# Kernel tuning notes

Measured on AMD Instinct MI355X. Metric: run time of the kernel, lower is better.

## Reference

```python
import jax, jax.numpy as jnp
import numpy as np


def setup_inputs() -> dict:
    key = jax.random.key(0)
    k1, k2, k3, k4, k5, k6 = jax.random.split(key, 6)
    B, N, D, H = 32, 4096, 256, 256
    return {
        "queries": jax.random.normal(k1, (B, N, D), dtype=jnp.float32),
        "keys": jax.random.normal(k2, (B, N, D), dtype=jnp.float32),
        "values": jax.random.normal(k3, (B, N, D), dtype=jnp.float32),
        "Wq": jax.random.normal(k4, (H, D), dtype=jnp.float32) * (1.0 / np.sqrt(D)),
        "Wk": jax.random.normal(k5, (H, D), dtype=jnp.float32) * (1.0 / np.sqrt(D)),
        "Wv": jax.random.normal(k6, (1, H), dtype=jnp.float32) * (1.0 / np.sqrt(H)),
    }


def reference(queries, keys, values, Wq, Wk, Wv):
    # Project queries and keys to hidden dim (torch Linear weight is [out, in])
    q = jnp.einsum('bnd,hd->bnh', queries, Wq)   # [B, N, H]
    k = jnp.einsum('bnd,hd->bnh', keys, Wk)      # [B, N, H]
    features = jnp.tanh(q + k)                   # [B, N, H]
    scores = jnp.einsum('bnh,oh->bno', features, Wv)  # [B, N, 1]
    alpha = jax.nn.softmax(scores, axis=1)       # softmax over N
    # dropout p=0 -> identity
    aggr_max = jnp.argmax(alpha, axis=1)         # [B, 1]
    out = jnp.sum(alpha * values, axis=1)        # [B, D]
    return (out, aggr_max)
```

## Files before the change

kernel.cpp:

```cpp
#include <hip/hip_runtime.h>

#define Bb 32
#define Nn 4096
#define Dd 256
#define Hh 256
#define NCH 32
#define CHUNK 128
#define NSTEPS 16

typedef __attribute__((ext_vector_type(8))) short bf16x8;
typedef __attribute__((ext_vector_type(4))) float f32x4;

__device__ __forceinline__ unsigned short bf16_rtn(float x) {
    unsigned int u = __float_as_uint(x);
    u += 0x7FFF + ((u >> 16) & 1);
    return (unsigned short)(u >> 16);
}
__device__ __forceinline__ float bf16_to_f(unsigned short b) {
    return __uint_as_float(((unsigned int)b) << 16);
}
__device__ __forceinline__ float fast_tanhf(float x) {
    float e = __expf(2.0f * x);
    return 1.0f - 2.0f / (e + 1.0f);
}

__device__ __forceinline__ void split8_store(short* hp, short* lp, f32x4 v0, f32x4 v1) {
    float xs[8] = {v0.x, v0.y, v0.z, v0.w, v1.x, v1.y, v1.z, v1.w};
    unsigned int hu[4], lu[4];
#pragma unroll
    for (int p = 0; p < 4; ++p) {
        unsigned int u0 = __float_as_uint(xs[2 * p]);
        unsigned int u1 = __float_as_uint(xs[2 * p + 1]);
        float r0 = xs[2 * p]     - __uint_as_float(u0 & 0xFFFF0000u);
        float r1 = xs[2 * p + 1] - __uint_as_float(u1 & 0xFFFF0000u);
        hu[p] = __builtin_amdgcn_perm(u1, u0, 0x07060302u);
        lu[p] = __builtin_amdgcn_perm(__float_as_uint(r1), __float_as_uint(r0), 0x07060302u);
    }
    *(uint4*)hp = make_uint4(hu[0], hu[1], hu[2], hu[3]);
    *(uint4*)lp = make_uint4(lu[0], lu[1], lu[2], lu[3]);
}

__global__ __launch_bounds__(256) void prep_w_kernel(
    const float* __restrict__ Wq, const float* __restrict__ Wk,
    short* __restrict__ Wh, short* __restrict__ Wl)
{
    const int g = blockIdx.x * 256 + threadIdx.x;
    const int s = g >> 10;
    const int j = (g >> 6) & 15;
    const int l = g & 63;
    const int n = j * 16 + (l & 15);
    const int k = s * 32 + (l >> 4) * 8;
    const float* src = (k < 256) ? (Wq + n * 256 + k) : (Wk + n * 256 + (k - 256));
    const f32x4 v0 = *(const f32x4*)src;
    const f32x4 v1 = *(const f32x4*)(src + 4);
    float xs[8] = {v0.x, v0.y, v0.z, v0.w, v1.x, v1.y, v1.z, v1.w};
    bf16x8 h8, l8;
#pragma unroll
    for (int e = 0; e < 8; ++e) {
        unsigned short hb = bf16_rtn(xs[e]);
        float rem = xs[e] - bf16_to_f(hb);
        h8[e] = (short)hb;
        l8[e] = (short)bf16_rtn(rem);
    }
    *(bf16x8*)&Wh[(size_t)g * 8] = h8;
    *(bf16x8*)&Wl[(size_t)g * 8] = l8;
}

__global__ __launch_bounds__(256, 2) void scores_mfma_kernel(
    const float* __restrict__ Q, const float* __restrict__ Kmat,
    const short* __restrict__ Wh, const short* __restrict__ Wl,
    const float* __restrict__ Wv, float* __restrict__ scores)
{
    __shared__ short Ah[2][4096];
    __shared__ short Al[2][4096];
    __shared__ float red[4][128];

    const int tid = threadIdx.x;
    const int lane = tid & 63;
    const int wave = tid >> 6;
    const size_t row0 = (size_t)blockIdx.x * 128;

    f32x4 acc[8][4];
#pragma unroll
    for (int m = 0; m < 8; ++m)
#pragma unroll
        for (int n = 0; n < 4; ++n) acc[m][n] = (f32x4){0.f, 0.f, 0.f, 0.f};

    float wv[4];
#pragma unroll
    for (int n = 0; n < 4; ++n) wv[n] = Wv[wave * 64 + n * 16 + (lane & 15)];

    const int r_s0 = ((tid >> 6) << 4) + (tid & 15);
    const int r_s1 = r_s0 + 64;
    const int k_s0 = ((tid >> 4) & 3) * 8;

    f32x4 a0, a1, a2, a3;

    auto issue_a = [&](int s) {
        const float* Asrc = (s < 8) ? Q : Kmat;
        const int kb = (s & 7) * 32 + k_s0;
        const float* p0 = Asrc + (row0 + r_s0) * Dd + kb;
        const float* p1 = Asrc + (row0 + r_s1) * Dd + kb;
        a0 = *(const f32x4*)p0; a1 = *(const f32x4*)(p0 + 4);
        a2 = *(const f32x4*)p1; a3 = *(const f32x4*)(p1 + 4);
    };
    auto issue_b = [&](int s, bf16x8 (&bh)[4], bf16x8 (&bl)[4]) {
#pragma unroll
        for (int n = 0; n < 4; ++n) {
            const size_t bo = ((size_t)(s * 16 + wave * 4 + n) * 64 + lane) * 8;
            bh[n] = *(const bf16x8*)(Wh + bo);
            bl[n] = *(const bf16x8*)(Wl + bo);
        }
    };
    auto split_store = [&](int buf) {
        split8_store(&Ah[buf][tid * 8], &Al[buf][tid * 8], a0, a1);
        split8_store(&Ah[buf][(tid + 256) * 8], &Al[buf][(tid + 256) * 8], a2, a3);
    };

    bf16x8 BAh[4], BAl[4], BBh[4], BBl[4];

    auto do_step = [&](int s, int cur, bf16x8 (&buh)[4], bf16x8 (&bul)[4],
                       bf16x8 (&bfh)[4], bf16x8 (&bfl)[4]) {
        const int sn = s + 1;
        if (sn < NSTEPS) {
            issue_a(sn);
            issue_b(sn, bfh, bfl);
        }
        __builtin_amdgcn_s_setprio(1);
#pragma unroll
        for (int m = 0; m < 8; ++m) {
            const bf16x8 ahm = *(const bf16x8*)&Ah[cur][(m * 64 + lane) * 8];
            const bf16x8 alm = *(const bf16x8*)&Al[cur][(m * 64 + lane) * 8];
#pragma unroll
            for (int n = 0; n < 4; ++n) {
                acc[m][n] = __builtin_amdgcn_mfma_f32_16x16x32_bf16(ahm, buh[n], acc[m][n], 0, 0, 0);
                acc[m][n] = __builtin_amdgcn_mfma_f32_16x16x32_bf16(alm, buh[n], acc[m][n], 0, 0, 0);
                acc[m][n] = __builtin_amdgcn_mfma_f32_16x16x32_bf16(ahm, bul[n], acc[m][n], 0, 0, 0);
            }
        }
        __builtin_amdgcn_s_setprio(0);
        if (sn < NSTEPS) split_store(cur ^ 1);
        __syncthreads();
    };

    issue_a(0);
    issue_b(0, BAh, BAl);
    split_store(0);
    __syncthreads();

    for (int s2 = 0; s2 < NSTEPS / 2; ++s2) {
        do_step(2 * s2,     0, BAh, BAl, BBh, BBl);
        do_step(2 * s2 + 1, 1, BBh, BBl, BAh, BAl);
    }

    const int q = lane >> 4;
    float rp[8][4];
#pragma unroll
    for (int m = 0; m < 8; ++m)
#pragma unroll
        for (int r = 0; r < 4; ++r) {
            float v = 0.f;
#pragma unroll
            for (int n = 0; n < 4; ++n)
                v += wv[n] * fast_tanhf(acc[m][n][r]);
            rp[m][r] = v;
        }
#pragma unroll
    for (int mask = 1; mask <= 8; mask <<= 1)
#pragma unroll
        for (int m = 0; m < 8; ++m)
#pragma unroll
            for (int r = 0; r < 4; ++r)
                rp[m][r] += __shfl_xor(rp[m][r], mask, 64);

    if ((lane & 15) == 0) {
#pragma unroll
        for (int m = 0; m < 8; ++m)
#pragma unroll
            for (int r = 0; r < 4; ++r)
                red[wave][m * 16 + q * 4 + r] = rp[m][r];
    }
    __syncthreads();
    if (tid < 128)
        scores[row0 + tid] = (red[0][tid] + red[1][tid]) + (red[2][tid] + red[3][tid]);
}

__global__ __launch_bounds__(256) void softmax_reduce_kernel(
    const float* __restrict__ scores, float* __restrict__ mbuf,
    float* __restrict__ zbuf, float* __restrict__ out)
{
    __shared__ float sv[256];
    __shared__ int si[256];
    const int b = blockIdx.x;
    const int tid = threadIdx.x;
    const float* sc = scores + (size_t)b * Nn;

    float best = -1e30f; int bi = 0;
    for (int j = 0; j < Nn / 256; ++j) {
        const int n = tid + j * 256;
        const float v = sc[n];
        if (v > best) { best = v; bi = n; }
    }
    sv[tid] = best; si[tid] = bi;
    __syncthreads();
    for (int off = 128; off > 0; off >>= 1) {
        if (tid < off) {
            const float v2 = sv[tid + off]; const int i2 = si[tid + off];
            if (v2 > sv[tid] || (v2 == sv[tid] && i2 < si[tid])) { sv[tid] = v2; si[tid] = i2; }
        }
        __syncthreads();
    }
    const float m = sv[0];
    const int amax = si[0];
    __syncthreads();

    float ssum = 0.f;
    for (int j = 0; j < Nn / 256; ++j) ssum += __expf(sc[tid + j * 256] - m);
    sv[tid] = ssum;
    __syncthreads();
    for (int off = 128; off > 0; off >>= 1) {
        if (tid < off) sv[tid] += sv[tid + off];
        __syncthreads();
    }
    if (tid == 0) {
        mbuf[b] = m;
        zbuf[b] = sv[0];
        out[(size_t)Bb * Dd + b] = (float)amax;
    }
}

__global__ __launch_bounds__(256) void partial_kernel(
    const float* __restrict__ V, const float* __restrict__ scores,
    const float* __restrict__ mbuf, float* __restrict__ part)
{
    __shared__ float e[CHUNK];
    const int c = blockIdx.x;
    const int b = blockIdx.y;
    const int tid = threadIdx.x;
    const float m = mbuf[b];
    if (tid < CHUNK)
        e[tid] = __expf(scores[(size_t)b * Nn + (size_t)c * CHUNK + tid] - m);
    __syncthreads();

    const float* vp = V + ((size_t)b * Nn + (size_t)c * CHUNK) * Dd + tid;
    float a0 = 0.f, a1 = 0.f, a2 = 0.f, a3 = 0.f;
    for (int n = 0; n < CHUNK; n += 4) {
        a0 = fmaf(e[n + 0], vp[(size_t)(n + 0) * Dd], a0);
        a1 = fmaf(e[n + 1], vp[(size_t)(n + 1) * Dd], a1);
        a2 = fmaf(e[n + 2], vp[(size_t)(n + 2) * Dd], a2);
        a3 = fmaf(e[n + 3], vp[(size_t)(n + 3) * Dd], a3);
    }
    part[((size_t)b * NCH + c) * Dd + tid] = ((a0 + a1) + (a2 + a3));
}

__global__ __launch_bounds__(256) void finalize_kernel(
    const float* __restrict__ part, const float* __restrict__ zbuf,
    float* __restrict__ out)
{
    const int b = blockIdx.x;
    const int tid = threadIdx.x;
    float s = 0.f;
#pragma unroll
    for (int c = 0; c < NCH; ++c) s += part[((size_t)b * NCH + c) * Dd + tid];
    out[(size_t)b * Dd + tid] = s / zbuf[b];
}

extern "C" void kernel_launch(void* const* d_in, const int* in_sizes, int n_in,
                              void* d_out, int out_size, void* d_ws, size_t ws_size,
                              hipStream_t stream) {
    const float* Q  = (const float*)d_in[0];
    const float* K  = (const float*)d_in[1];
    const float* V  = (const float*)d_in[2];
    const float* Wq = (const float*)d_in[3];
    const float* Wk = (const float*)d_in[4];
    const float* Wv = (const float*)d_in[5];
    float* out = (float*)d_out;

    char* wsb = (char*)d_ws;
    short* Wh     = (short*)(wsb);
    short* Wl     = (short*)(wsb + 262144);
    float* scores = (float*)(wsb + 524288);
    float* mbuf   = (float*)(wsb + 1048576);
    float* zbuf   = (float*)(wsb + 1048576 + 128);
    float* part   = (float*)(wsb + 1048576 + 256);

    prep_w_kernel<<<dim3(64), dim3(256), 0, stream>>>(Wq, Wk, Wh, Wl);
    scores_mfma_kernel<<<dim3((Bb * Nn) / 128), dim3(256), 0, stream>>>(Q, K, Wh, Wl, Wv, scores);
    softmax_reduce_kernel<<<dim3(Bb), dim3(256), 0, stream>>>(scores, mbuf, zbuf, out);
    partial_kernel<<<dim3(NCH, Bb), dim3(256), 0, stream>>>(V, scores, mbuf, part);
    finalize_kernel<<<dim3(Bb), dim3(256), 0, stream>>>(part, zbuf, out);
}
```

Measured before the change: 139.5 us.

## Deepen A-tile prefetch to two steps ahead with triple-buffered LDS

Measured after the change: 132.5 us. 1.05x faster.

```diff
diff --git a/kernel.cpp b/kernel.cpp
--- a/kernel.cpp
+++ b/kernel.cpp
@@ -71,8 +71,8 @@
     const short* __restrict__ Wh, const short* __restrict__ Wl,
     const float* __restrict__ Wv, float* __restrict__ scores)
 {
-    __shared__ short Ah[2][4096];
-    __shared__ short Al[2][4096];
+    __shared__ short Ah[3][4096];
+    __shared__ short Al[3][4096];
     __shared__ float red[4][128];
 
     const int tid = threadIdx.x;
@@ -94,17 +94,29 @@
     const int r_s1 = r_s0 + 64;
     const int k_s0 = ((tid >> 4) & 3) * 8;
 
-    f32x4 a0, a1, a2, a3;
-
-    auto issue_a = [&](int s) {
+    f32x4 pA0, pA1, pA2, pA3;
+    f32x4 qA0, qA1, qA2, qA3;
+    bf16x8 bh[4], bl[4];
+
+    auto issue_aP = [&](int s) {
+        if (s >= NSTEPS) return;
         const float* Asrc = (s < 8) ? Q : Kmat;
         const int kb = (s & 7) * 32 + k_s0;
         const float* p0 = Asrc + (row0 + r_s0) * Dd + kb;
         const float* p1 = Asrc + (row0 + r_s1) * Dd + kb;
-        a0 = *(const f32x4*)p0; a1 = *(const f32x4*)(p0 + 4);
-        a2 = *(const f32x4*)p1; a3 = *(const f32x4*)(p1 + 4);
-    };
-    auto issue_b = [&](int s, bf16x8 (&bh)[4], bf16x8 (&bl)[4]) {
+        pA0 = *(const f32x4*)p0; pA1 = *(const f32x4*)(p0 + 4);
+        pA2 = *(const f32x4*)p1; pA3 = *(const f32x4*)(p1 + 4);
+    };
+    auto issue_aQ = [&](int s) {
+        if (s >= NSTEPS) return;
+        const float* Asrc = (s < 8) ? Q : Kmat;
+        const int kb = (s & 7) * 32 + k_s0;
+        const float* p0 = Asrc + (row0 + r_s0) * Dd + kb;
+        const float* p1 = Asrc + (row0 + r_s1) * Dd + kb;
+        qA0 = *(const f32x4*)p0; qA1 = *(const f32x4*)(p0 + 4);
+        qA2 = *(const f32x4*)p1; qA3 = *(const f32x4*)(p1 + 4);
+    };
+    auto issue_b = [&](int s) {
 #pragma unroll
         for (int n = 0; n < 4; ++n) {
             const size_t bo = ((size_t)(s * 16 + wave * 4 + n) * 64 + lane) * 8;
@@ -112,45 +124,51 @@
             bl[n] = *(const bf16x8*)(Wl + bo);
         }
     };
-    auto split_store = [&](int buf) {
-        split8_store(&Ah[buf][tid * 8], &Al[buf][tid * 8], a0, a1);
-        split8_store(&Ah[buf][(tid + 256) * 8], &Al[buf][(tid + 256) * 8], a2, a3);
-    };
-
-    bf16x8 BAh[4], BAl[4], BBh[4], BBl[4];
-
-    auto do_step = [&](int s, int cur, bf16x8 (&buh)[4], bf16x8 (&bul)[4],
-                       bf16x8 (&bfh)[4], bf16x8 (&bfl)[4]) {
-        const int sn = s + 1;
-        if (sn < NSTEPS) {
-            issue_a(sn);
-            issue_b(sn, bfh, bfl);
-        }
+    auto splitP = [&](int buf) {
+        split8_store(&Ah[buf][tid * 8], &Al[buf][tid * 8], pA0, pA1);
+        split8_store(&Ah[buf][(tid + 256) * 8], &Al[buf][(tid + 256) * 8], pA2, pA3);
+    };
+    auto splitQ = [&](int buf) {
+        split8_store(&Ah[buf][tid * 8], &Al[buf][tid * 8], qA0, qA1);
+        split8_store(&Ah[buf][(tid + 256) * 8], &Al[buf][(tid + 256) * 8], qA2, qA3);
+    };
+    auto cluster = [&](int rb) {
+        const short* ahb = &Ah[rb][0];
+        const short* alb = &Al[rb][0];
         __builtin_amdgcn_s_setprio(1);
 #pragma unroll
         for (int m = 0; m < 8; ++m) {
-            const bf16x8 ahm = *(const bf16x8*)&Ah[cur][(m * 64 + lane) * 8];
-            const bf16x8 alm = *(const bf16x8*)&Al[cur][(m * 64 + lane) * 8];
+            const bf16x8 ahm = *(const bf16x8*)&ahb[(m * 64 + lane) * 8];
+            const bf16x8 alm = *(const bf16x8*)&alb[(m * 64 + lane) * 8];
 #pragma unroll
             for (int n = 0; n < 4; ++n) {
-                acc[m][n] = __builtin_amdgcn_mfma_f32_16x16x32_bf16(ahm, buh[n], acc[m][n], 0, 0, 0);
-                acc[m][n] = __builtin_amdgcn_mfma_f32_16x16x32_bf16(alm, buh[n], acc[m][n], 0, 0, 0);
-                acc[m][n] = __builtin_amdgcn_mfma_f32_16x16x32_bf16(ahm, bul[n], acc[m][n], 0, 0, 0);
+                acc[m][n] = __builtin_amdgcn_mfma_f32_16x16x32_bf16(ahm, bh[n], acc[m][n], 0, 0, 0);
+                acc[m][n] = __builtin_amdgcn_mfma_f32_16x16x32_bf16(alm, bh[n], acc[m][n], 0, 0, 0);
+                acc[m][n] = __builtin_amdgcn_mfma_f32_16x16x32_bf16(ahm, bl[n], acc[m][n], 0, 0, 0);
             }
         }
         __builtin_amdgcn_s_setprio(0);
-        if (sn < NSTEPS) split_store(cur ^ 1);
+    };
+
+    issue_aP(0);
+    issue_aQ(1);
+    splitP(0);
+    __syncthreads();
+
+    int rb = 0;
+    for (int s2 = 0; s2 < NSTEPS / 2; ++s2) {
+        const int s = 2 * s2;
+        issue_b(s);
+        issue_aP(s + 2);
+        cluster(rb);
+        if (s + 1 < NSTEPS) splitQ(rb == 2 ? 0 : rb + 1);
         __syncthreads();
-    };
-
-    issue_a(0);
-    issue_b(0, BAh, BAl);
-    split_store(0);
-    __syncthreads();
-
-    for (int s2 = 0; s2 < NSTEPS / 2; ++s2) {
-        do_step(2 * s2,     0, BAh, BAl, BBh, BBl);
-        do_step(2 * s2 + 1, 1, BBh, BBl, BAh, BAl);
+        issue_b(s + 1);
+        issue_aQ(s + 3);
+        cluster(rb == 2 ? 0 : rb + 1);
+        if (s + 2 < NSTEPS) splitP(rb >= 1 ? rb - 1 : rb + 2);
+        __syncthreads();
+        rb = (rb >= 1) ? rb - 1 : rb + 2;
     }
 
     const int q = lane >> 4;
```
